# Optimization experiments

Measured on AMD Instinct MI355X. Metric: run time of the kernel, lower is better.

The kernel has to match this reference:

```python
import jax, jax.numpy as jnp
import numpy as np

C = 64
N_H = 4
N_WIN = 16
WIN_L = 8   # compressor window length (overlapped)
WIN_S = 4   # compressor stride -> T//4 blocks


def _rms(x, eps=1e-6):
    return x * jax.lax.rsqrt(jnp.mean(x * x, axis=-1, keepdims=True) + eps)


def _rope(x, negate=False):
    # x: (..., L, D); rotate-half RoPE over positions 0..L-1
    L, D = x.shape[-2], x.shape[-1]
    half = D // 2
    inv_freq = 1.0 / (10000.0 ** (jnp.arange(half, dtype=x.dtype) / half))
    ang = jnp.arange(L, dtype=x.dtype)[:, None] * inv_freq  # (L, half)
    if negate:
        ang = -ang
    cos, sin = jnp.cos(ang), jnp.sin(ang)
    x1, x2 = x[..., :half], x[..., half:]
    return jnp.concatenate([x1 * cos - x2 * sin, x1 * sin + x2 * cos], axis=-1)


def _compress(H, W):
    # overlapped token compressor: windows of WIN_L, stride WIN_S, zero-pad tail
    B, T, d = H.shape
    Tc = T // WIN_S
    Hp = jnp.pad(H, ((0, 0), (0, WIN_L - WIN_S), (0, 0)))
    idx = WIN_S * jnp.arange(Tc)[:, None] + jnp.arange(WIN_L)[None, :]  # (Tc, WIN_L)
    win = Hp[:, idx]                       # (B, Tc, WIN_L, d)
    return win.reshape(B, Tc, WIN_L * d) @ W  # (B, Tc, out)


def setup_inputs() -> dict:
    key = jax.random.key(0)
    ks = jax.random.split(key, 11)
    B, T, d = 2, 2048, 256

    def w(k, shape, fan):
        return jax.random.normal(k, shape, jnp.float32) / np.float32(np.sqrt(fan))

    H = jax.random.normal(ks[0], (B, T, d), jnp.float32)
    return {
        'H': H,
        'Wc_comp': w(ks[1], (WIN_L * d, C), WIN_L * d),
        'Wc_idx': w(ks[2], (WIN_L * d, 32), WIN_L * d),
        'W_DQ': w(ks[3], (d, 64), d),
        'W_IUQ': w(ks[4], (64, 4 * 32), 64),
        'W_w': w(ks[5], (64, 4), 64),
        'W_Q': w(ks[6], (d, N_H * C), d),
        'W_KV': w(ks[7], (d, C), d),
        'g_q': jnp.ones((N_H, C), jnp.float32),
        'g_k': jnp.ones((C,), jnp.float32),
        'g_v': jnp.ones((C,), jnp.float32),
        'Wg0': w(ks[8], (2 * C, 64), 2 * C),
        'bg0': jnp.zeros((64,), jnp.float32),
        'Wg1': w(ks[9], (2 * C, 64), 2 * C),
        'bg1': jnp.zeros((64,), jnp.float32),
        'Wout': w(ks[10], (128, d), 128),
        'bout': jnp.zeros((d,), jnp.float32),
    }


def reference(H, Wc_comp, Wc_idx, W_DQ, W_IUQ, W_w, W_Q, W_KV,
              g_q, g_k, g_v, Wg0, bg0, Wg1, bg1, Wout, bout):
    B, T, d = H.shape
    Tc = T // 4
    k_top = min(8, Tc)

    # ---- lightning indexer ----
    H_dc = H @ W_DQ                                   # (B,T,64)
    Q_I = (H_dc @ W_IUQ).reshape(B, T, 4, 32)         # (B,T,4,32)
    W_Iw = (H_dc @ W_w)[..., None]                    # (B,T,4,1)
    K_I = _compress(H, Wc_idx)                        # (B,Tc,32)
    dot = jnp.einsum('bthc,bsc->bths', Q_I, K_I)      # (B,T,4,Tc)
    I_ts = (W_Iw * jax.nn.relu(dot)).sum(axis=2)      # (B,T,Tc)

    t = jnp.arange(T)[:, None]
    s = jnp.arange(Tc)[None, :]
    mask_I = jnp.where(4 * s <= t, 0.0, -jnp.inf)     # (T,Tc) causal over blocks
    _, topk_idx = jax.lax.top_k(I_ts + mask_I, k_top)  # (B,T,k)
    bI = jnp.arange(B)[:, None, None]
    tI = jnp.arange(T)[None, :, None]
    M_comp = jnp.full((B, T, Tc), -jnp.inf).at[bI, tI, topk_idx].set(0.0)

    # ---- compressed + sliding KV ----
    KV = jnp.concatenate([_compress(H, Wc_comp), H @ W_KV], axis=1)  # (B,Tc+T,C)

    Q = (H @ W_Q).reshape(B, T, N_H, C).transpose(0, 2, 1, 3)        # (B,nh,T,C)
    Q = _rms(Q) * g_q[None, :, None, :]
    K = _rms(KV) * g_k
    V = _rms(KV) * g_v
    Q = _rope(Q)
    K = _rope(K)
    V = _rope(V)

    S = jnp.einsum('bhtc,bsc->bhts', Q, K) / np.float32(np.sqrt(C))  # (B,nh,T,Tc+T)

    S_comp = S[..., :Tc] + M_comp[:, None]
    rel = t - jnp.arange(T)[None, :]
    mask_slide = jnp.where((rel >= 0) & (rel < N_WIN), 0.0, -jnp.inf)  # (T,T)
    S_slide = S[..., Tc:] + mask_slide

    P = jax.nn.softmax(jnp.concatenate([S_comp, S_slide], axis=-1), axis=-1)
    O = jnp.einsum('bhts,bsc->bhtc', P, V)            # (B,nh,T,C)
    O = _rope(O, negate=True)

    O0 = O[:, :2].transpose(0, 2, 1, 3).reshape(B, T, 2 * C)
    O1 = O[:, 2:].transpose(0, 2, 1, 3).reshape(B, T, 2 * C)
    p_all = jnp.concatenate([O0 @ Wg0 + bg0, O1 @ Wg1 + bg1], axis=-1)
    return p_all @ Wout + bout
```

## Files before the change

### kernel.cpp

```cpp
#include <hip/hip_runtime.h>
#include <hip/hip_bf16.h>
#include <math.h>

#define T_DIM 2048
#define B_DIM 2
#define D_DIM 256
#define TC 512
#define KV_LEN 2560

typedef __attribute__((ext_vector_type(8))) short bf16x8;
typedef __attribute__((ext_vector_type(4))) float f32x4;
typedef unsigned short ush;

__device__ __forceinline__ float wave_sum64(float v) {
#pragma unroll
    for (int off = 32; off > 0; off >>= 1) v += __shfl_xor(v, off, 64);
    return v;
}

__device__ __forceinline__ float rope_angle(int pos, int j) {
    float inv = powf(10000.0f, -(float)j * (1.0f / 32.0f));
    return (float)pos * inv;
}

__global__ __launch_bounds__(256) void k_prep(
    const float* __restrict__ H, const float* __restrict__ W_Q,
    const float* __restrict__ W_KV, const float* __restrict__ W_DQ,
    const float* __restrict__ W_IUQ, const float* __restrict__ W_w,
    const float* __restrict__ Wc_comp, const float* __restrict__ Wc_idx,
    const float* __restrict__ Wg0, const float* __restrict__ bg0,
    const float* __restrict__ Wg1, const float* __restrict__ bg1,
    const float* __restrict__ Wout, const float* __restrict__ bout,
    ush* __restrict__ Ap, ush* __restrict__ Ac,
    ush* __restrict__ Bp, ush* __restrict__ Bc,
    ush* __restrict__ Bo, float* __restrict__ biascomb)
{
    int gid = blockIdx.x * 256 + threadIdx.x;
    float vals[8];
    ush* dst;
    bool lo_part;

    if (gid < 262144) {
        int tile = gid >> 10;
        int c = (gid >> 6) & 15;
        int l = gid & 63;
        int bt = tile * 16 + (l & 15);
        int kb = (c & 7) * 32 + (l >> 4) * 8;
        const float* src = H + (size_t)bt * 256 + kb;
#pragma unroll
        for (int j = 0; j < 8; ++j) vals[j] = src[j];
        lo_part = (c >= 8);
        dst = Ap + (size_t)gid * 8;
    } else if (gid < 786432) {
        int g = gid - 262144;
        int tile = g >> 13;
        int c = (g >> 6) & 127;
        int l = g & 63;
        int m = tile * 16 + (l & 15);
        int s = m & 511;
        int b = m >> 9;
        int k2b = (c & 63) * 32 + (l >> 4) * 8;
        int r4 = 4 * s + (k2b >> 8);
        int col = k2b & 255;
        if (r4 < T_DIM) {
            const float* src = H + ((size_t)b * T_DIM + r4) * 256 + col;
#pragma unroll
            for (int j = 0; j < 8; ++j) vals[j] = src[j];
        } else {
#pragma unroll
            for (int j = 0; j < 8; ++j) vals[j] = 0.f;
        }
        lo_part = (c >= 64);
        dst = Ac + (size_t)g * 8;
    } else if (gid < 819200) {
        int g = gid - 786432;
        int tile = g >> 10;
        int c = (g >> 6) & 15;
        int l = g & 63;
        int n = tile * 16 + (l & 15);
        int kb = (c & 7) * 32 + (l >> 4) * 8;
#pragma unroll
        for (int j = 0; j < 8; ++j) {
            int k = kb + j;
            float w;
            if (n < 256)      w = W_Q[(size_t)k * 256 + n];
            else if (n < 320) w = W_KV[(size_t)k * 64 + (n - 256)];
            else if (n < 448) {
                w = 0.f;
                for (int i = 0; i < 64; ++i)
                    w = fmaf(W_DQ[(size_t)k * 64 + i], W_IUQ[(size_t)i * 128 + (n - 320)], w);
            } else if (n < 452) {
                w = 0.f;
                for (int i = 0; i < 64; ++i)
                    w = fmaf(W_DQ[(size_t)k * 64 + i], W_w[(size_t)i * 4 + (n - 448)], w);
            } else {
                w = 0.f;
            }
            vals[j] = w;
        }
        lo_part = (c >= 8);
        dst = Bp + (size_t)g * 8;
    } else if (gid < 868352) {
        int g = gid - 819200;
        int tile = g >> 13;
        int c = (g >> 6) & 127;
        int l = g & 63;
        int n = tile * 16 + (l & 15);
        int k2b = (c & 63) * 32 + (l >> 4) * 8;
#pragma unroll
        for (int j = 0; j < 8; ++j) {
            int k = k2b + j;
            vals[j] = (n < 64) ? Wc_comp[(size_t)k * 64 + n]
                               : Wc_idx[(size_t)k * 32 + (n - 64)];
        }
        lo_part = (c >= 64);
        dst = Bc + (size_t)g * 8;
    } else if (gid < 933888) {
        int g = gid - 868352;
        int k = g >> 8;
        int n = g & 255;
        float acc = 0.f;
        if (k < 128) {
            for (int i = 0; i < 64; ++i)
                acc = fmaf(Wg0[k * 64 + i], Wout[(size_t)i * 256 + n], acc);
        } else {
            for (int i = 0; i < 64; ++i)
                acc = fmaf(Wg1[(k - 128) * 64 + i], Wout[(size_t)(64 + i) * 256 + n], acc);
        }
        __hip_bfloat16 hb = __float2bfloat16(acc);
        float hif = __bfloat162float(hb);
        __hip_bfloat16 lb = __float2bfloat16(acc - hif);
        int tile = n >> 4;
        int chi = k >> 5;
        int lane2 = (n & 15) + 16 * ((k >> 3) & 3);
        int j = k & 7;
        Bo[(size_t)(tile * 16 + chi) * 512 + lane2 * 8 + j] = *(ush*)&hb;
        Bo[(size_t)(tile * 16 + chi + 8) * 512 + lane2 * 8 + j] = *(ush*)&lb;
        return;
    } else if (gid < 934144) {
        int n = gid - 933888;
        float acc = bout[n];
        for (int i = 0; i < 64; ++i) {
            acc = fmaf(bg0[i], Wout[(size_t)i * 256 + n], acc);
            acc = fmaf(bg1[i], Wout[(size_t)(64 + i) * 256 + n], acc);
        }
        biascomb[n] = acc;
        return;
    } else {
        return;
    }

    bf16x8 out8;
#pragma unroll
    for (int j = 0; j < 8; ++j) {
        float x = vals[j];
        __hip_bfloat16 hb = __float2bfloat16(x);
        if (!lo_part) {
            out8[j] = *(short*)&hb;
        } else {
            float hif = __bfloat162float(hb);
            __hip_bfloat16 lb = __float2bfloat16(x - hif);
            out8[j] = *(short*)&lb;
        }
    }
    *(bf16x8*)dst = out8;
}

__global__ __launch_bounds__(64) void k_mfma(
    const ush* __restrict__ Ap, const ush* __restrict__ Ac,
    const ush* __restrict__ Bp, const ush* __restrict__ Bc,
    float* __restrict__ Pre, float* __restrict__ Prec_part)
{
    int lane = threadIdx.x;
    int mrow = lane & 15;
    int q = lane >> 4;

    if (blockIdx.x < 512) {
        int p = blockIdx.x;
        int m0 = (p >> 2) * 32;
        int n0 = (p & 3) * 128;
        int at0 = (m0 >> 4) * 16;
        int bt0n = (n0 >> 4) * 16;

        f32x4 acc[2][8];
#pragma unroll
        for (int mt = 0; mt < 2; ++mt)
#pragma unroll
            for (int nt = 0; nt < 8; ++nt) acc[mt][nt] = (f32x4){0.f, 0.f, 0.f, 0.f};

        for (int c = 0; c < 8; ++c) {
            bf16x8 ahi[2], alo[2], bhi[8], blo[8];
#pragma unroll
            for (int mt = 0; mt < 2; ++mt) {
                ahi[mt] = *(const bf16x8*)(Ap + (size_t)((at0 + mt * 16) + c) * 512 + lane * 8);
                alo[mt] = *(const bf16x8*)(Ap + (size_t)((at0 + mt * 16) + 8 + c) * 512 + lane * 8);
            }
#pragma unroll
            for (int nt = 0; nt < 8; ++nt) {
                bhi[nt] = *(const bf16x8*)(Bp + (size_t)((bt0n + nt * 16) + c) * 512 + lane * 8);
                blo[nt] = *(const bf16x8*)(Bp + (size_t)((bt0n + nt * 16) + 8 + c) * 512 + lane * 8);
            }
#pragma unroll
            for (int mt = 0; mt < 2; ++mt)
#pragma unroll
                for (int nt = 0; nt < 8; ++nt) {
                    acc[mt][nt] = __builtin_amdgcn_mfma_f32_16x16x32_bf16(ahi[mt], bhi[nt], acc[mt][nt], 0, 0, 0);
                    acc[mt][nt] = __builtin_amdgcn_mfma_f32_16x16x32_bf16(ahi[mt], blo[nt], acc[mt][nt], 0, 0, 0);
                    acc[mt][nt] = __builtin_amdgcn_mfma_f32_16x16x32_bf16(alo[mt], bhi[nt], acc[mt][nt], 0, 0, 0);
                }
        }

#pragma unroll
        for (int mt = 0; mt < 2; ++mt)
#pragma unroll
            for (int nt = 0; nt < 8; ++nt)
#pragma unroll
                for (int reg = 0; reg < 4; ++reg)
                    Pre[(size_t)(m0 + 16 * mt + 4 * q + reg) * 512 + n0 + 16 * nt + mrow] =
                        acc[mt][nt][reg];
    } else {
        int cb = blockIdx.x - 512;
        int m0 = (cb >> 2) * 32;
        int q4 = cb & 3;
        int at0 = (m0 >> 4) * 128;

        f32x4 acc[2][6];
#pragma unroll
        for (int mt = 0; mt < 2; ++mt)
#pragma unroll
            for (int nt = 0; nt < 6; ++nt) acc[mt][nt] = (f32x4){0.f, 0.f, 0.f, 0.f};

        for (int cl = 0; cl < 16; ++cl) {
            int c = q4 * 16 + cl;
            bf16x8 ahi[2], alo[2], bhi[6], blo[6];
#pragma unroll
            for (int mt = 0; mt < 2; ++mt) {
                ahi[mt] = *(const bf16x8*)(Ac + (size_t)((at0 + mt * 128) + c) * 512 + lane * 8);
                alo[mt] = *(const bf16x8*)(Ac + (size_t)((at0 + mt * 128) + 64 + c) * 512 + lane * 8);
            }
#pragma unroll
            for (int nt = 0; nt < 6; ++nt) {
                bhi[nt] = *(const bf16x8*)(Bc + (size_t)(nt * 128 + c) * 512 + lane * 8);
                blo[nt] = *(const bf16x8*)(Bc + (size_t)(nt * 128 + 64 + c) * 512 + lane * 8);
            }
#pragma unroll
            for (int mt = 0; mt < 2; ++mt)
#pragma unroll
                for (int nt = 0; nt < 6; ++nt) {
                    acc[mt][nt] = __builtin_amdgcn_mfma_f32_16x16x32_bf16(ahi[mt], bhi[nt], acc[mt][nt], 0, 0, 0);
                    acc[mt][nt] = __builtin_amdgcn_mfma_f32_16x16x32_bf16(ahi[mt], blo[nt], acc[mt][nt], 0, 0, 0);
                    acc[mt][nt] = __builtin_amdgcn_mfma_f32_16x16x32_bf16(alo[mt], bhi[nt], acc[mt][nt], 0, 0, 0);
                }
        }

        float* dst = Prec_part + (size_t)q4 * (1024 * 96);
#pragma unroll
        for (int mt = 0; mt < 2; ++mt)
#pragma unroll
            for (int nt = 0; nt < 6; ++nt)
#pragma unroll
                for (int reg = 0; reg < 4; ++reg)
                    dst[(size_t)(m0 + 16 * mt + 4 * q + reg) * 96 + 16 * nt + mrow] =
                        acc[mt][nt][reg];
    }
}

__global__ __launch_bounds__(256) void k_epi(
    const float* __restrict__ Pre, const float* __restrict__ Prec_part,
    const float* __restrict__ g_q, const float* __restrict__ g_k,
    const float* __restrict__ g_v,
    float* __restrict__ Qr, float* __restrict__ KIbuf,
    float* __restrict__ Kbuf, float* __restrict__ Vbuf)
{
    int tid = threadIdx.x;
    int wv = tid >> 6;
    int lane = tid & 63;

    if (blockIdx.x < 1024) {
        int bt = blockIdx.x * 4 + wv;
        int b = bt >> 11;
        int t = bt & 2047;

        const float* pr = Pre + (size_t)bt * 512;
        int j = lane & 31;
        float s_t, c_t;
        sincosf(rope_angle(t, j), &s_t, &c_t);

#pragma unroll
        for (int r = 0; r < 4; ++r) {
            float qv = pr[r * 64 + lane];
            float ss = wave_sum64(qv * qv);
            float sc = rsqrtf(ss * (1.0f / 64.0f) + 1e-6f);
            float qq = qv * sc * g_q[r * 64 + lane];
            float prt = __shfl_xor(qq, 32, 64);
            float o = (lane < 32) ? fmaf(qq, c_t, -prt * s_t)
                                  : fmaf(prt, s_t, qq * c_t);
            Qr[(size_t)bt * 256 + r * 64 + lane] = o;
        }
        {
            float kvv = pr[256 + lane];
            float ss = wave_sum64(kvv * kvv);
            float sc = rsqrtf(ss * (1.0f / 64.0f) + 1e-6f);
            float kk = kvv * sc * g_k[lane];
            float vv = kvv * sc * g_v[lane];
            int pos = TC + t;
            float s_p, c_p;
            sincosf(rope_angle(pos, j), &s_p, &c_p);
            float pk = __shfl_xor(kk, 32, 64);
            float pv = __shfl_xor(vv, 32, 64);
            float ko = (lane < 32) ? fmaf(kk, c_p, -pk * s_p) : fmaf(pk, s_p, kk * c_p);
            float vo = (lane < 32) ? fmaf(vv, c_p, -pv * s_p) : fmaf(pv, s_p, vv * c_p);
            size_t off = ((size_t)b * KV_LEN + pos) * 64 + lane;
            Kbuf[off] = ko;
            Vbuf[off] = vo;
        }
    } else {
        int sg = (blockIdx.x - 1024) * 4 + wv;
        int b = sg >> 9;
        int s = sg & 511;

        const float* p0 = Prec_part + (size_t)sg * 96;
        float kvv = p0[lane] + p0[98304 + lane] + p0[2 * 98304 + lane] + p0[3 * 98304 + lane];

        float ss = wave_sum64(kvv * kvv);
        float sc = rsqrtf(ss * (1.0f / 64.0f) + 1e-6f);
        float kk = kvv * sc * g_k[lane];
        float vv = kvv * sc * g_v[lane];
        int j = lane & 31;
        float sa, ca;
        sincosf(rope_angle(s, j), &sa, &ca);
        float pk = __shfl_xor(kk, 32, 64);
        float pv = __shfl_xor(vv, 32, 64);
        float ko = (lane < 32) ? fmaf(kk, ca, -pk * sa) : fmaf(pk, sa, kk * ca);
        float vo = (lane < 32) ? fmaf(vv, ca, -pv * sa) : fmaf(pv, sa, vv * ca);
        size_t off = ((size_t)b * KV_LEN + s) * 64 + lane;
        Kbuf[off] = ko;
        Vbuf[off] = vo;

        if (lane < 32) {
            float a = p0[64 + lane] + p0[98304 + 64 + lane] +
                      p0[2 * 98304 + 64 + lane] + p0[3 * 98304 + 64 + lane];
            KIbuf[((size_t)b * TC + s) * 32 + lane] = a;
        }
    }
}

__global__ __launch_bounds__(256) void k_score_topk(
    const float* __restrict__ Pre, const float* __restrict__ KIbuf,
    int* __restrict__ topk)
{
    int tid = threadIdx.x;
    int wv = tid >> 6;
    int lane = tid & 63;
    int bt0 = blockIdx.x * 4;
    int bt = bt0 + wv;
    int b = bt >> 11;
    int t = bt & 2047;

    __shared__ float sQ[4][128];
    __shared__ float sw[4][4];
    __shared__ float sKI[64 * 33];

    const float* pr = Pre + (size_t)bt * 512;
    sQ[wv][lane] = pr[320 + lane];
    sQ[wv][64 + lane] = pr[384 + lane];
    if (lane < 4) sw[wv][lane] = pr[448 + lane];

    const float* KIb = KIbuf + (size_t)b * TC * 32;
    int smax = t >> 2;
    int smax_blk = ((bt0 + 3) & 2047) >> 2;

    float vals[8];
#pragma unroll
    for (int r = 0; r < 8; ++r) vals[r] = -INFINITY;

    for (int r = 0; r < 8; ++r) {
        if (r * 64 > smax_blk) break;
        __syncthreads();
        for (int i = tid; i < 512; i += 256) {
            int row = i >> 3;
            int cseg = (i & 7) * 4;
            float4 v = *(const float4*)(KIb + (size_t)(r * 64 + row) * 32 + cseg);
            float* dstp = &sKI[row * 33 + cseg];
            dstp[0] = v.x; dstp[1] = v.y; dstp[2] = v.z; dstp[3] = v.w;
        }
        __syncthreads();

        int s = r * 64 + lane;
        if (s <= smax) {
            float dd0 = 0.f, dd1 = 0.f, dd2 = 0.f, dd3 = 0.f;
#pragma unroll
            for (int c = 0; c < 32; ++c) {
                float kv = sKI[lane * 33 + c];
                dd0 = fmaf(sQ[wv][c], kv, dd0);
                dd1 = fmaf(sQ[wv][32 + c], kv, dd1);
                dd2 = fmaf(sQ[wv][64 + c], kv, dd2);
                dd3 = fmaf(sQ[wv][96 + c], kv, dd3);
            }
            vals[r] = sw[wv][0] * fmaxf(dd0, 0.f) + sw[wv][1] * fmaxf(dd1, 0.f) +
                      sw[wv][2] * fmaxf(dd2, 0.f) + sw[wv][3] * fmaxf(dd3, 0.f);
        }
    }

    unsigned consumed = 0u;
    for (int k2 = 0; k2 < 8; ++k2) {
        float bv = -INFINITY;
        int bi = 0x7fffffff;
#pragma unroll
        for (int r = 0; r < 8; ++r) {
            if (!(consumed & (1u << r))) {
                int s = lane + 64 * r;
                float v = vals[r];
                if (v > bv || (v == bv && s < bi)) { bv = v; bi = s; }
            }
        }
#pragma unroll
        for (int off = 1; off < 64; off <<= 1) {
            float ov = __shfl_xor(bv, off, 64);
            int oi = __shfl_xor(bi, off, 64);
            if (ov > bv || (ov == bv && oi < bi)) { bv = ov; bi = oi; }
        }
        if ((bi & 63) == lane) consumed |= 1u << (bi >> 6);
        if (lane == 0) topk[(size_t)bt * 8 + k2] = bi;
    }
}

__global__ __launch_bounds__(1024) void k_attn(
    const float* __restrict__ Qr, const float* __restrict__ Kbuf,
    const float* __restrict__ Vbuf, const int* __restrict__ topk,
    float* __restrict__ Obuf)
{
    int tid = threadIdx.x;
    int lt = tid >> 8;
    int t256 = tid & 255;
    int h = t256 >> 6;
    int lane = tid & 63;
    int bt = blockIdx.x * 4 + lt;
    int b = bt >> 11;
    int t = bt & 2047;

    __shared__ float sKV[4][48 * 65];
    __shared__ float sQ[4][256];
    __shared__ int sPos[4][24];
    __shared__ float sP[4][4][24];

    sQ[lt][t256] = Qr[(size_t)bt * 256 + t256];
    if (t256 < 8) {
        sPos[lt][t256] = topk[(size_t)bt * 8 + t256];
    } else if (t256 < 24) {
        int rel = t256 - 8;
        int sp = t - rel;
        sPos[lt][t256] = (sp >= 0) ? (TC + sp) : -1;
    }
    __syncthreads();

    for (int i = t256; i < 768; i += 256) {
        int row = i >> 4;
        int seg = (i & 15) << 2;
        int key = (row < 24) ? row : row - 24;
        int pos = sPos[lt][key];
        if (pos >= 0) {
            const float* src = ((row < 24) ? Kbuf : Vbuf) +
                               ((size_t)b * KV_LEN + pos) * 64 + seg;
            float4 v = *(const float4*)src;
            float* dst = &sKV[lt][row * 65 + seg];
            dst[0] = v.x; dst[1] = v.y; dst[2] = v.z; dst[3] = v.w;
        }
    }
    __syncthreads();

    float scv = -INFINITY;
    if (lane < 24) {
        int pos = sPos[lt][lane];
        if (pos >= 0) {
            float dd = 0.f;
#pragma unroll
            for (int c = 0; c < 64; ++c)
                dd = fmaf(sQ[lt][h * 64 + c], sKV[lt][lane * 65 + c], dd);
            scv = dd * 0.125f;
        }
    }
    float m = scv;
#pragma unroll
    for (int off = 1; off < 64; off <<= 1) m = fmaxf(m, __shfl_xor(m, off, 64));
    float p = expf(scv - m);
    if (scv == -INFINITY) p = 0.f;
    float l = p;
#pragma unroll
    for (int off = 1; off < 64; off <<= 1) l += __shfl_xor(l, off, 64);
    p /= l;
    if (lane < 24) sP[lt][h][lane] = p;

    float o = 0.f;
#pragma unroll
    for (int j2 = 0; j2 < 24; ++j2) {
        int pos = sPos[lt][j2];
        if (pos >= 0)
            o = fmaf(sP[lt][h][j2], sKV[lt][(24 + j2) * 65 + lane], o);
    }

    int j = lane & 31;
    float sa, ca;
    sincosf(rope_angle(t, j), &sa, &ca);
    float prt = __shfl_xor(o, 32, 64);
    float oo = (lane < 32) ? fmaf(o, ca, prt * sa) : fmaf(-prt, sa, o * ca);
    Obuf[(size_t)bt * 256 + h * 64 + lane] = oo;
}

__global__ __launch_bounds__(64) void k_out(
    const float* __restrict__ Obuf, const ush* __restrict__ Bo,
    const float* __restrict__ biascomb, float* __restrict__ out)
{
    int lane = threadIdx.x;
    int mrow = lane & 15;
    int q = lane >> 4;
    int p = blockIdx.x;
    int m0 = (p >> 2) * 32;
    int n0 = (p & 3) * 64;
    int bt0n = (n0 >> 4) * 16;

    f32x4 acc[2][4];
#pragma unroll
    for (int mt = 0; mt < 2; ++mt)
#pragma unroll
        for (int nt = 0; nt < 4; ++nt) acc[mt][nt] = (f32x4){0.f, 0.f, 0.f, 0.f};

    for (int c = 0; c < 8; ++c) {
        bf16x8 ahi[2], alo[2], bhi[4], blo[4];
#pragma unroll
        for (int mt = 0; mt < 2; ++mt) {
            const float* src = Obuf + (size_t)(m0 + 16 * mt + mrow) * 256 + c * 32 + 8 * q;
            float4 x0 = *(const float4*)src;
            float4 x1 = *(const float4*)(src + 4);
            float xs[8] = {x0.x, x0.y, x0.z, x0.w, x1.x, x1.y, x1.z, x1.w};
#pragma unroll
            for (int j = 0; j < 8; ++j) {
                __hip_bfloat16 hb = __float2bfloat16(xs[j]);
                float hif = __bfloat162float(hb);
                __hip_bfloat16 lb = __float2bfloat16(xs[j] - hif);
                ahi[mt][j] = *(short*)&hb;
                alo[mt][j] = *(short*)&lb;
            }
        }
#pragma unroll
        for (int nt = 0; nt < 4; ++nt) {
            bhi[nt] = *(const bf16x8*)(Bo + (size_t)((bt0n + nt * 16) + c) * 512 + lane * 8);
            blo[nt] = *(const bf16x8*)(Bo + (size_t)((bt0n + nt * 16) + 8 + c) * 512 + lane * 8);
        }
#pragma unroll
        for (int mt = 0; mt < 2; ++mt)
#pragma unroll
            for (int nt = 0; nt < 4; ++nt) {
                acc[mt][nt] = __builtin_amdgcn_mfma_f32_16x16x32_bf16(ahi[mt], bhi[nt], acc[mt][nt], 0, 0, 0);
                acc[mt][nt] = __builtin_amdgcn_mfma_f32_16x16x32_bf16(ahi[mt], blo[nt], acc[mt][nt], 0, 0, 0);
                acc[mt][nt] = __builtin_amdgcn_mfma_f32_16x16x32_bf16(alo[mt], bhi[nt], acc[mt][nt], 0, 0, 0);
            }
    }

#pragma unroll
    for (int mt = 0; mt < 2; ++mt)
#pragma unroll
        for (int nt = 0; nt < 4; ++nt) {
            float bia = biascomb[n0 + 16 * nt + mrow];
#pragma unroll
            for (int reg = 0; reg < 4; ++reg)
                out[(size_t)(m0 + 16 * mt + 4 * q + reg) * 256 + n0 + 16 * nt + mrow] =
                    acc[mt][nt][reg] + bia;
        }
}

extern "C" void kernel_launch(void* const* d_in, const int* in_sizes, int n_in,
                              void* d_out, int out_size, void* d_ws, size_t ws_size,
                              hipStream_t stream) {
    const float* H       = (const float*)d_in[0];
    const float* Wc_comp = (const float*)d_in[1];
    const float* Wc_idx  = (const float*)d_in[2];
    const float* W_DQ    = (const float*)d_in[3];
    const float* W_IUQ   = (const float*)d_in[4];
    const float* W_w     = (const float*)d_in[5];
    const float* W_Q     = (const float*)d_in[6];
    const float* W_KV    = (const float*)d_in[7];
    const float* g_q     = (const float*)d_in[8];
    const float* g_k     = (const float*)d_in[9];
    const float* g_v     = (const float*)d_in[10];
    const float* Wg0     = (const float*)d_in[11];
    const float* bg0     = (const float*)d_in[12];
    const float* Wg1     = (const float*)d_in[13];
    const float* bg1     = (const float*)d_in[14];
    const float* Wout    = (const float*)d_in[15];
    const float* bout    = (const float*)d_in[16];

    float* ws = (float*)d_ws;
    float* Qr   = ws;
    float* KI   = ws + 1048576;
    float* Kb   = ws + 1081344;
    float* Vb   = ws + 1409024;
    float* Pre  = ws + 1736704;
    float* Prec = ws + 3833856;
    float* Obuf = ws + 4227072;
    int* topkb  = (int*)(ws + 5275648);
    ush* Ap = (ush*)(ws + 5308416);
    ush* Ac = (ush*)(ws + 6356992);
    ush* Bp = (ush*)(ws + 8454144);
    ush* Bc = (ush*)(ws + 8585216);
    ush* Bo = (ush*)(ws + 8781824);
    float* biascomb = ws + 8847360;

    float* outp = (float*)d_out;

    hipLaunchKernelGGL(k_prep, dim3(3649), dim3(256), 0, stream,
                       H, W_Q, W_KV, W_DQ, W_IUQ, W_w, Wc_comp, Wc_idx,
                       Wg0, bg0, Wg1, bg1, Wout, bout,
                       Ap, Ac, Bp, Bc, Bo, biascomb);
    hipLaunchKernelGGL(k_mfma, dim3(640), dim3(64), 0, stream,
                       Ap, Ac, Bp, Bc, Pre, Prec);
    hipLaunchKernelGGL(k_epi, dim3(1280), dim3(256), 0, stream,
                       Pre, Prec, g_q, g_k, g_v, Qr, KI, Kb, Vb);
    hipLaunchKernelGGL(k_score_topk, dim3(1024), dim3(256), 0, stream,
                       Pre, KI, topkb);
    hipLaunchKernelGGL(k_attn, dim3(1024), dim3(1024), 0, stream,
                       Qr, Kb, Vb, topkb, Obuf);
    hipLaunchKernelGGL(k_out, dim3(512), dim3(64), 0, stream,
                       Obuf, Bo, biascomb, outp);
}
```

Baseline: 176.6 us.

## Fuse index scoring, top-k selection and attention into one kernel; move Q norm/RoPE in

Merges k_score_topk and k_attn into a single 1024-thread kernel. Each block now scores the compressed indexer keys with four waves per token, does a two-level top-k (a per-wave top-8, then a merge of the 32 candidates), and feeds the selected positions straight into the attention step through shared memory. The Q RMSNorm and RoPE move from k_epi into the fused kernel, removing the Qr and topk global buffers and one launch. k_epi shrinks to K/V work with four tokens per wave. The trade-off is higher shared-memory use and more synchronization inside the fused block.

```diff
diff --git a/kernel.cpp b/kernel.cpp
--- a/kernel.cpp
+++ b/kernel.cpp
@@ -267,38 +267,21 @@
 
 __global__ __launch_bounds__(256) void k_epi(
     const float* __restrict__ Pre, const float* __restrict__ Prec_part,
-    const float* __restrict__ g_q, const float* __restrict__ g_k,
-    const float* __restrict__ g_v,
-    float* __restrict__ Qr, float* __restrict__ KIbuf,
-    float* __restrict__ Kbuf, float* __restrict__ Vbuf)
+    const float* __restrict__ g_k, const float* __restrict__ g_v,
+    float* __restrict__ KIbuf, float* __restrict__ Kbuf, float* __restrict__ Vbuf)
 {
     int tid = threadIdx.x;
     int wv = tid >> 6;
     int lane = tid & 63;
-
-    if (blockIdx.x < 1024) {
-        int bt = blockIdx.x * 4 + wv;
-        int b = bt >> 11;
-        int t = bt & 2047;
-
-        const float* pr = Pre + (size_t)bt * 512;
-        int j = lane & 31;
-        float s_t, c_t;
-        sincosf(rope_angle(t, j), &s_t, &c_t);
-
-#pragma unroll
-        for (int r = 0; r < 4; ++r) {
-            float qv = pr[r * 64 + lane];
-            float ss = wave_sum64(qv * qv);
-            float sc = rsqrtf(ss * (1.0f / 64.0f) + 1e-6f);
-            float qq = qv * sc * g_q[r * 64 + lane];
-            float prt = __shfl_xor(qq, 32, 64);
-            float o = (lane < 32) ? fmaf(qq, c_t, -prt * s_t)
-                                  : fmaf(prt, s_t, qq * c_t);
-            Qr[(size_t)bt * 256 + r * 64 + lane] = o;
-        }
-        {
-            float kvv = pr[256 + lane];
+    int j = lane & 31;
+
+    if (blockIdx.x < 256) {
+#pragma unroll
+        for (int tt = 0; tt < 4; ++tt) {
+            int bt = blockIdx.x * 16 + wv * 4 + tt;
+            int b = bt >> 11;
+            int t = bt & 2047;
+            float kvv = Pre[(size_t)bt * 512 + 256 + lane];
             float ss = wave_sum64(kvv * kvv);
             float sc = rsqrtf(ss * (1.0f / 64.0f) + 1e-6f);
             float kk = kvv * sc * g_k[lane];
@@ -315,7 +298,7 @@
             Vbuf[off] = vo;
         }
     } else {
-        int sg = (blockIdx.x - 1024) * 4 + wv;
+        int sg = (blockIdx.x - 256) * 4 + wv;
         int b = sg >> 9;
         int s = sg & 511;
 
@@ -326,7 +309,6 @@
         float sc = rsqrtf(ss * (1.0f / 64.0f) + 1e-6f);
         float kk = kvv * sc * g_k[lane];
         float vv = kvv * sc * g_v[lane];
-        int j = lane & 31;
         float sa, ca;
         sincosf(rope_angle(s, j), &sa, &ca);
         float pk = __shfl_xor(kk, 32, 64);
@@ -345,115 +327,125 @@
     }
 }
 
-__global__ __launch_bounds__(256) void k_score_topk(
+__global__ __launch_bounds__(1024) void k_fused(
     const float* __restrict__ Pre, const float* __restrict__ KIbuf,
-    int* __restrict__ topk)
+    const float* __restrict__ Kbuf, const float* __restrict__ Vbuf,
+    const float* __restrict__ g_q, float* __restrict__ Obuf)
 {
     int tid = threadIdx.x;
     int wv = tid >> 6;
     int lane = tid & 63;
+    int lt = tid >> 8;
+    int t256 = tid & 255;
     int bt0 = blockIdx.x * 4;
-    int bt = bt0 + wv;
-    int b = bt >> 11;
-    int t = bt & 2047;
-
-    __shared__ float sQ[4][128];
-    __shared__ float sw[4][4];
-    __shared__ float sKI[64 * 33];
-
-    const float* pr = Pre + (size_t)bt * 512;
-    sQ[wv][lane] = pr[320 + lane];
-    sQ[wv][64 + lane] = pr[384 + lane];
-    if (lane < 4) sw[wv][lane] = pr[448 + lane];
-
+    int b = bt0 >> 11;
+
+    int tg = wv >> 2;
+    int sub = wv & 3;
+    int t_tg = (bt0 + tg) & 2047;
+
+    __shared__ float sBig[12480];
+    __shared__ float sQ[4][256];
+    __shared__ float sQI[4][128];
+    __shared__ float swq[4][4];
+    __shared__ int   sPos[4][24];
+    __shared__ float sP[4][4][24];
+    __shared__ float sCandV[4][4][8];
+    __shared__ int   sCandI[4][4][8];
+
+    {
+        int bt_l = bt0 + lt;
+        if (t256 < 128) sQI[lt][t256] = Pre[(size_t)bt_l * 512 + 320 + t256];
+        else if (t256 < 132) swq[lt][t256 - 128] = Pre[(size_t)bt_l * 512 + 448 + (t256 - 128)];
+        if (t256 >= 8 && t256 < 24) {
+            int rel = t256 - 8;
+            int tl = bt_l & 2047;
+            int sp = tl - rel;
+            sPos[lt][t256] = (sp >= 0) ? (TC + sp) : -1;
+        }
+    }
+
+    int smax = t_tg >> 2;
+    int smax_blk = ((bt0 + 3) & 2047) >> 2;
     const float* KIb = KIbuf + (size_t)b * TC * 32;
-    int smax = t >> 2;
-    int smax_blk = ((bt0 + 3) & 2047) >> 2;
-
-    float vals[8];
-#pragma unroll
-    for (int r = 0; r < 8; ++r) vals[r] = -INFINITY;
-
-    for (int r = 0; r < 8; ++r) {
-        if (r * 64 > smax_blk) break;
+
+    float vals[2] = {-INFINITY, -INFINITY};
+
+    for (int p = 0; p < 2; ++p) {
+        if (p * 256 > smax_blk) break;
         __syncthreads();
-        for (int i = tid; i < 512; i += 256) {
+        for (int i = tid; i < 2048; i += 1024) {
             int row = i >> 3;
             int cseg = (i & 7) * 4;
-            float4 v = *(const float4*)(KIb + (size_t)(r * 64 + row) * 32 + cseg);
-            float* dstp = &sKI[row * 33 + cseg];
-            dstp[0] = v.x; dstp[1] = v.y; dstp[2] = v.z; dstp[3] = v.w;
+            float4 v = *(const float4*)(KIb + (size_t)(p * 256 + row) * 32 + cseg);
+            float* d = &sBig[row * 33 + cseg];
+            d[0] = v.x; d[1] = v.y; d[2] = v.z; d[3] = v.w;
         }
         __syncthreads();
 
-        int s = r * 64 + lane;
+        int s = p * 256 + sub * 64 + lane;
         if (s <= smax) {
+            int row = sub * 64 + lane;
             float dd0 = 0.f, dd1 = 0.f, dd2 = 0.f, dd3 = 0.f;
 #pragma unroll
             for (int c = 0; c < 32; ++c) {
-                float kv = sKI[lane * 33 + c];
-                dd0 = fmaf(sQ[wv][c], kv, dd0);
-                dd1 = fmaf(sQ[wv][32 + c], kv, dd1);
-                dd2 = fmaf(sQ[wv][64 + c], kv, dd2);
-                dd3 = fmaf(sQ[wv][96 + c], kv, dd3);
-            }
-            vals[r] = sw[wv][0] * fmaxf(dd0, 0.f) + sw[wv][1] * fmaxf(dd1, 0.f) +
-                      sw[wv][2] * fmaxf(dd2, 0.f) + sw[wv][3] * fmaxf(dd3, 0.f);
-        }
-    }
-
-    unsigned consumed = 0u;
-    for (int k2 = 0; k2 < 8; ++k2) {
-        float bv = -INFINITY;
-        int bi = 0x7fffffff;
-#pragma unroll
-        for (int r = 0; r < 8; ++r) {
-            if (!(consumed & (1u << r))) {
-                int s = lane + 64 * r;
-                float v = vals[r];
-                if (v > bv || (v == bv && s < bi)) { bv = v; bi = s; }
-            }
-        }
-#pragma unroll
-        for (int off = 1; off < 64; off <<= 1) {
-            float ov = __shfl_xor(bv, off, 64);
-            int oi = __shfl_xor(bi, off, 64);
-            if (ov > bv || (ov == bv && oi < bi)) { bv = ov; bi = oi; }
-        }
-        if ((bi & 63) == lane) consumed |= 1u << (bi >> 6);
-        if (lane == 0) topk[(size_t)bt * 8 + k2] = bi;
-    }
-}
-
-__global__ __launch_bounds__(1024) void k_attn(
-    const float* __restrict__ Qr, const float* __restrict__ Kbuf,
-    const float* __restrict__ Vbuf, const int* __restrict__ topk,
-    float* __restrict__ Obuf)
-{
-    int tid = threadIdx.x;
-    int lt = tid >> 8;
-    int t256 = tid & 255;
-    int h = t256 >> 6;
-    int lane = tid & 63;
-    int bt = blockIdx.x * 4 + lt;
-    int b = bt >> 11;
-    int t = bt & 2047;
-
-    __shared__ float sKV[4][48 * 65];
-    __shared__ float sQ[4][256];
-    __shared__ int sPos[4][24];
-    __shared__ float sP[4][4][24];
-
-    sQ[lt][t256] = Qr[(size_t)bt * 256 + t256];
-    if (t256 < 8) {
-        sPos[lt][t256] = topk[(size_t)bt * 8 + t256];
-    } else if (t256 < 24) {
-        int rel = t256 - 8;
-        int sp = t - rel;
-        sPos[lt][t256] = (sp >= 0) ? (TC + sp) : -1;
+                float kv = sBig[row * 33 + c];
+                dd0 = fmaf(sQI[tg][c], kv, dd0);
+                dd1 = fmaf(sQI[tg][32 + c], kv, dd1);
+                dd2 = fmaf(sQI[tg][64 + c], kv, dd2);
+                dd3 = fmaf(sQI[tg][96 + c], kv, dd3);
+            }
+            vals[p] = swq[tg][0] * fmaxf(dd0, 0.f) + swq[tg][1] * fmaxf(dd1, 0.f) +
+                      swq[tg][2] * fmaxf(dd2, 0.f) + swq[tg][3] * fmaxf(dd3, 0.f);
+        }
+    }
+
+    {
+        unsigned consumed = 0u;
+        for (int k2 = 0; k2 < 8; ++k2) {
+            float bv = -INFINITY;
+            int bi = 0x7fffffff;
+#pragma unroll
+            for (int rr = 0; rr < 2; ++rr) {
+                if (!(consumed & (1u << rr))) {
+                    int s = rr * 256 + sub * 64 + lane;
+                    float v = vals[rr];
+                    if (v > bv || (v == bv && s < bi)) { bv = v; bi = s; }
+                }
+            }
+#pragma unroll
+            for (int off = 1; off < 64; off <<= 1) {
+                float ov = __shfl_xor(bv, off, 64);
+                int oi = __shfl_xor(bi, off, 64);
+                if (ov > bv || (ov == bv && oi < bi)) { bv = ov; bi = oi; }
+            }
+            if ((bi & 255) == sub * 64 + lane) consumed |= 1u << (bi >> 8);
+            if (lane == 0) { sCandV[tg][sub][k2] = bv; sCandI[tg][sub][k2] = bi; }
+        }
     }
     __syncthreads();
 
+    if (sub == 0) {
+        float mv; int mi;
+        if (lane < 32) { mv = sCandV[tg][lane >> 3][lane & 7]; mi = sCandI[tg][lane >> 3][lane & 7]; }
+        else           { mv = -INFINITY; mi = 0x7fffffff; }
+        bool cons = false;
+        for (int k2 = 0; k2 < 8; ++k2) {
+            float bv = cons ? -INFINITY : mv;
+            int bi = cons ? 0x7fffffff : mi;
+#pragma unroll
+            for (int off = 1; off < 64; off <<= 1) {
+                float ov = __shfl_xor(bv, off, 64);
+                int oi = __shfl_xor(bi, off, 64);
+                if (ov > bv || (ov == bv && oi < bi)) { bv = ov; bi = oi; }
+            }
+            if (!cons && bi == mi) cons = true;
+            if (lane == 0) sPos[tg][k2] = bi;
+        }
+    }
+    __syncthreads();
+
+    float (*sKV)[48 * 65] = (float (*)[48 * 65])sBig;
     for (int i = t256; i < 768; i += 256) {
         int row = i >> 4;
         int seg = (i & 15) << 2;
@@ -463,9 +455,24 @@
             const float* src = ((row < 24) ? Kbuf : Vbuf) +
                                ((size_t)b * KV_LEN + pos) * 64 + seg;
             float4 v = *(const float4*)src;
-            float* dst = &sKV[lt][row * 65 + seg];
-            dst[0] = v.x; dst[1] = v.y; dst[2] = v.z; dst[3] = v.w;
-        }
+            float* d = &sKV[lt][row * 65 + seg];
+            d[0] = v.x; d[1] = v.y; d[2] = v.z; d[3] = v.w;
+        }
+    }
+
+    int h = t256 >> 6;
+    int t_l = (bt0 + lt) & 2047;
+    int j = lane & 31;
+    float sa, ca;
+    sincosf(rope_angle(t_l, j), &sa, &ca);
+    {
+        float qraw = Pre[(size_t)(bt0 + lt) * 512 + h * 64 + lane];
+        float ss = wave_sum64(qraw * qraw);
+        float sc = rsqrtf(ss * (1.0f / 64.0f) + 1e-6f);
+        float qv = qraw * sc * g_q[h * 64 + lane];
+        float pa = __shfl_xor(qv, 32, 64);
+        float qf = (lane < 32) ? fmaf(qv, ca, -pa * sa) : fmaf(pa, sa, qv * ca);
+        sQ[lt][h * 64 + lane] = qf;
     }
     __syncthreads();
 
@@ -483,13 +490,13 @@
     float m = scv;
 #pragma unroll
     for (int off = 1; off < 64; off <<= 1) m = fmaxf(m, __shfl_xor(m, off, 64));
-    float p = expf(scv - m);
-    if (scv == -INFINITY) p = 0.f;
-    float l = p;
-#pragma unroll
-    for (int off = 1; off < 64; off <<= 1) l += __shfl_xor(l, off, 64);
-    p /= l;
-    if (lane < 24) sP[lt][h][lane] = p;
+    float p2 = expf(scv - m);
+    if (scv == -INFINITY) p2 = 0.f;
+    float l2 = p2;
+#pragma unroll
+    for (int off = 1; off < 64; off <<= 1) l2 += __shfl_xor(l2, off, 64);
+    p2 /= l2;
+    if (lane < 24) sP[lt][h][lane] = p2;
 
     float o = 0.f;
 #pragma unroll
@@ -499,12 +506,9 @@
             o = fmaf(sP[lt][h][j2], sKV[lt][(24 + j2) * 65 + lane], o);
     }
 
-    int j = lane & 31;
-    float sa, ca;
-    sincosf(rope_angle(t, j), &sa, &ca);
     float prt = __shfl_xor(o, 32, 64);
     float oo = (lane < 32) ? fmaf(o, ca, prt * sa) : fmaf(-prt, sa, o * ca);
-    Obuf[(size_t)bt * 256 + h * 64 + lane] = oo;
+    Obuf[(size_t)(bt0 + lt) * 256 + h * 64 + lane] = oo;
 }
 
 __global__ __launch_bounds__(64) void k_out(
@@ -591,20 +595,18 @@
     const float* bout    = (const float*)d_in[16];
 
     float* ws = (float*)d_ws;
-    float* Qr   = ws;
-    float* KI   = ws + 1048576;
-    float* Kb   = ws + 1081344;
-    float* Vb   = ws + 1409024;
-    float* Pre  = ws + 1736704;
-    float* Prec = ws + 3833856;
-    float* Obuf = ws + 4227072;
-    int* topkb  = (int*)(ws + 5275648);
-    ush* Ap = (ush*)(ws + 5308416);
-    ush* Ac = (ush*)(ws + 6356992);
-    ush* Bp = (ush*)(ws + 8454144);
-    ush* Bc = (ush*)(ws + 8585216);
-    ush* Bo = (ush*)(ws + 8781824);
-    float* biascomb = ws + 8847360;
+    float* KI   = ws;
+    float* Kb   = ws + 32768;
+    float* Vb   = ws + 360448;
+    float* Pre  = ws + 688128;
+    float* Prec = ws + 2785280;
+    float* Obuf = ws + 3178496;
+    ush* Ap = (ush*)(ws + 4227072);
+    ush* Ac = (ush*)(ws + 5275648);
+    ush* Bp = (ush*)(ws + 7372800);
+    ush* Bc = (ush*)(ws + 7503872);
+    ush* Bo = (ush*)(ws + 7700480);
+    float* biascomb = ws + 7766016;
 
     float* outp = (float*)d_out;
 
@@ -614,12 +616,10 @@
                        Ap, Ac, Bp, Bc, Bo, biascomb);
     hipLaunchKernelGGL(k_mfma, dim3(640), dim3(64), 0, stream,
                        Ap, Ac, Bp, Bc, Pre, Prec);
-    hipLaunchKernelGGL(k_epi, dim3(1280), dim3(256), 0, stream,
-                       Pre, Prec, g_q, g_k, g_v, Qr, KI, Kb, Vb);
-    hipLaunchKernelGGL(k_score_topk, dim3(1024), dim3(256), 0, stream,
-                       Pre, KI, topkb);
-    hipLaunchKernelGGL(k_attn, dim3(1024), dim3(1024), 0, stream,
-                       Qr, Kb, Vb, topkb, Obuf);
+    hipLaunchKernelGGL(k_epi, dim3(512), dim3(256), 0, stream,
+                       Pre, Prec, g_k, g_v, KI, Kb, Vb);
+    hipLaunchKernelGGL(k_fused, dim3(1024), dim3(1024), 0, stream,
+                       Pre, KI, Kb, Vb, g_q, Obuf);
     hipLaunchKernelGGL(k_out, dim3(512), dim3(64), 0, stream,
                        Obuf, Bo, biascomb, outp);
 }
```

Result: slower. 198.1 us (+12.2%).
